# Kernel tuning notes

Hardware: AMD Instinct MI355X
Metric: run time of the kernel (lower is better)

## Reference

```python
import jax, jax.numpy as jnp
import numpy as np

HEAD_DIM = 128
N_HEADS = 32
N_KV = 8
EPS = 1e-6


def setup_inputs() -> dict:
    key = jax.random.key(0)
    ks = jax.random.split(key, 8)
    B, S, H = 1, 2048, 2560
    hidden_states = jax.random.normal(ks[0], (B, S, H), dtype=jnp.float32)
    # rotary embeddings (any values work for a math reference)
    pos = jnp.arange(S, dtype=jnp.float32)[:, None]
    inv_freq = 1.0 / (10000.0 ** (jnp.arange(0, HEAD_DIM, 2, dtype=jnp.float32) / HEAD_DIM))
    ang = pos * inv_freq[None, :]            # [S, HEAD_DIM/2]
    emb = jnp.concatenate([ang, ang], axis=-1)  # [S, HEAD_DIM]
    cos = jnp.cos(emb)[None]                 # [1, S, HEAD_DIM]
    sin = jnp.sin(emb)[None]
    sc = 0.02
    Wq = jax.random.normal(ks[1], (N_HEADS * HEAD_DIM, H), dtype=jnp.float32) * sc
    Wk = jax.random.normal(ks[2], (N_KV * HEAD_DIM, H), dtype=jnp.float32) * sc
    Wv = jax.random.normal(ks[3], (N_KV * HEAD_DIM, H), dtype=jnp.float32) * sc
    Wo = jax.random.normal(ks[4], (H, N_HEADS * HEAD_DIM), dtype=jnp.float32) * sc
    q_norm_w = jnp.ones((HEAD_DIM,), dtype=jnp.float32)
    k_norm_w = jnp.ones((HEAD_DIM,), dtype=jnp.float32)
    return dict(hidden_states=hidden_states, cos=cos, sin=sin,
                Wq=Wq, Wk=Wk, Wv=Wv, Wo=Wo,
                q_norm_w=q_norm_w, k_norm_w=k_norm_w)


def _rms_norm(x, w):
    var = jnp.mean(x * x, axis=-1, keepdims=True)
    return x * jax.lax.rsqrt(var + EPS) * w


def _rotate_half(x):
    x1, x2 = jnp.split(x, 2, axis=-1)
    return jnp.concatenate([-x2, x1], axis=-1)


def reference(hidden_states, cos, sin, Wq, Wk, Wv, Wo, q_norm_w, k_norm_w):
    B, S, H = hidden_states.shape
    scale = HEAD_DIM ** -0.5
    # projections -> [B, heads, S, D]
    q = (hidden_states @ Wq.T).reshape(B, S, N_HEADS, HEAD_DIM)
    k = (hidden_states @ Wk.T).reshape(B, S, N_KV, HEAD_DIM)
    v = (hidden_states @ Wv.T).reshape(B, S, N_KV, HEAD_DIM)
    q = _rms_norm(q, q_norm_w).transpose(0, 2, 1, 3)   # [B, 32, S, D]
    k = _rms_norm(k, k_norm_w).transpose(0, 2, 1, 3)   # [B, 8, S, D]
    v = v.transpose(0, 2, 1, 3)
    # RoPE (cos/sin broadcast over heads via [:, None])
    c = cos[:, None]
    s = sin[:, None]
    q = q * c + _rotate_half(q) * s
    k = k * c + _rotate_half(k) * s
    # GQA: expand kv heads (repeat_kv)
    rep = N_HEADS // N_KV
    k = jnp.repeat(k, rep, axis=1)  # [B, 32, S, D]
    v = jnp.repeat(v, rep, axis=1)
    # causal SDPA (prefill => is_causal=True, full-length cache)
    scores = jnp.einsum('bhqd,bhkd->bhqk', q, k) * scale
    causal = jnp.tril(jnp.ones((S, S), dtype=bool))
    scores = jnp.where(causal, scores, jnp.finfo(scores.dtype).min)
    probs = jax.nn.softmax(scores, axis=-1)
    out = jnp.einsum('bhqk,bhkd->bhqd', probs, v)      # [B, 32, S, D]
    out = out.transpose(0, 2, 1, 3).reshape(B, S, N_HEADS * HEAD_DIM)
    return out @ Wo.T
```

## Files before the change

### kernel.cpp

```cpp
#include <hip/hip_runtime.h>
#include <hip/hip_bf16.h>

#define S_LEN   2048
#define HID     2560
#define NH      32
#define NKV     8
#define HD      128
#define QDIM    (NH*HD)
#define KVDIM   (NKV*HD)

typedef __attribute__((ext_vector_type(8))) short short8;
typedef __attribute__((ext_vector_type(4))) float f32x4;

__device__ __forceinline__ unsigned short f2bf(float f) {
    unsigned u = __float_as_uint(f);
    u += 0x7fffu + ((u >> 16) & 1u);
    return (unsigned short)(u >> 16);
}
__device__ __forceinline__ float bf2f(unsigned short s) {
    return __uint_as_float(((unsigned)s) << 16);
}
__device__ __forceinline__ unsigned pk2bf(float a, float b) {
    __hip_bfloat162 h = __float22bfloat162_rn(make_float2(a, b));
    union { __hip_bfloat162 h; unsigned u; } c; c.h = h; return c.u;
}
__device__ __forceinline__ void gload16(const void* g, void* l) {
    __builtin_amdgcn_global_load_lds(
        (const __attribute__((address_space(1))) unsigned int*)g,
        (__attribute__((address_space(3))) unsigned int*)l, 16, 0, 0);
}

#define N4_HS  (S_LEN*HID/4)
#define N4_WQ  (QDIM*HID/4)
#define N4_WKV (KVDIM*HID/4)
__global__ __launch_bounds__(256) void cvt4(
    const float* __restrict__ hs, const float* __restrict__ Wq,
    const float* __restrict__ Wk, const float* __restrict__ Wv,
    unsigned short* __restrict__ hsB, unsigned short* __restrict__ WqB,
    unsigned short* __restrict__ WkB, unsigned short* __restrict__ WvB)
{
    int i = blockIdx.x * 256 + threadIdx.x;
    const float* s; unsigned short* d;
    if (i < N4_HS)                          { s = hs; d = hsB; }
    else if (i < N4_HS + N4_WQ)             { i -= N4_HS; s = Wq; d = WqB; }
    else if (i < N4_HS + N4_WQ + N4_WKV)    { i -= N4_HS + N4_WQ; s = Wk; d = WkB; }
    else                                    { i -= N4_HS + N4_WQ + N4_WKV; s = Wv; d = WvB; }
    float4 v = ((const float4*)s)[i];
    uint2 o;
    o.x = pk2bf(v.x, v.y); o.y = pk2bf(v.z, v.w);
    ((uint2*)d)[i] = o;
}

__global__ __launch_bounds__(256) void cvt_f32_bf16(
    const float* __restrict__ s, unsigned short* __restrict__ d, int n4)
{
    int i = blockIdx.x * 256 + threadIdx.x;
    if (i >= n4) return;
    float4 v = ((const float4*)s)[i];
    uint2 o;
    o.x = pk2bf(v.x, v.y); o.y = pk2bf(v.z, v.w);
    ((uint2*)d)[i] = o;
}

#define STG_A(b, h, t) do {                                                  \
    _Pragma("unroll")                                                        \
    for (int c_ = 0; c_ < 2; c_++) {                                         \
        int r_ = c_*128 + (h)*64 + (tid >> 3);                               \
        int cg_ = (tid & 7) ^ (r_ & 7);                                      \
        gload16(Ag + (size_t)(rowA0 + r_) * HID + (size_t)(t)*64 + cg_*8,    \
                &As[b][r_*64 + (tid & 7)*8]);                                \
    } } while (0)

#define STG_B(b, h, t) do {                                                  \
    _Pragma("unroll")                                                        \
    for (int c_ = 0; c_ < 2; c_++) {                                         \
        int r_ = c_*128 + ((tid >> 8) << 6) + (h)*32 + ((tid >> 3) & 31);    \
        int cg_ = (tid & 7) ^ (r_ & 7);                                      \
        gload16(Bg + (size_t)(rowB0 + r_) * HID + (size_t)(t)*64 + cg_*8,    \
                &Bs[b][r_*64 + (tid & 7)*8]);                                \
    } } while (0)

#define PHASE(b, rh, ch, STAGE_STMT, WV) do {                                \
    short8 af_[4][2], bf_[2][2];                                             \
    _Pragma("unroll")                                                        \
    for (int i_ = 0; i_ < 4; i_++) {                                         \
        int row_ = wr + (rh)*64 + i_*16 + l15;                               \
        _Pragma("unroll")                                                    \
        for (int kk_ = 0; kk_ < 2; kk_++)                                    \
            af_[i_][kk_] = *(const short8*)                                  \
                &As[b][row_*64 + (((kk_*4 + l4) ^ sw8))*8];                  \
    }                                                                        \
    _Pragma("unroll")                                                        \
    for (int j_ = 0; j_ < 2; j_++) {                                         \
        int row_ = wc + (ch)*32 + j_*16 + l15;                               \
        _Pragma("unroll")                                                    \
        for (int kk_ = 0; kk_ < 2; kk_++)                                    \
            bf_[j_][kk_] = *(const short8*)                                  \
                &Bs[b][row_*64 + (((kk_*4 + l4) ^ sw8))*8];                  \
    }                                                                        \
    STAGE_STMT;                                                              \
    asm volatile("s_barrier" ::: "memory");                                  \
    asm volatile("s_waitcnt lgkmcnt(0)" ::: "memory");                       \
    __builtin_amdgcn_s_setprio(1);                                           \
    _Pragma("unroll")                                                        \
    for (int kk_ = 0; kk_ < 2; kk_++)                                        \
        _Pragma("unroll")                                                    \
        for (int i_ = 0; i_ < 4; i_++)                                       \
            _Pragma("unroll")                                                \
            for (int j_ = 0; j_ < 2; j_++)                                   \
                acc[(rh)*4 + i_][(ch)*2 + j_] =                              \
                    __builtin_amdgcn_mfma_f32_16x16x32_bf16(                 \
                        af_[i_][kk_], bf_[j_][kk_],                          \
                        acc[(rh)*4 + i_][(ch)*2 + j_], 0, 0, 0);             \
    __builtin_amdgcn_s_setprio(0);                                           \
    if ((WV) == 1) {                                                         \
        if (p2v) asm volatile("s_waitcnt vmcnt(4)" ::: "memory");            \
        else     asm volatile("s_waitcnt vmcnt(0)" ::: "memory");            \
    } else if ((WV) == 2) {                                                  \
        asm volatile("s_waitcnt vmcnt(4)" ::: "memory");                     \
    }                                                                        \
    asm volatile("s_barrier" ::: "memory");                                  \
} while (0)

__global__ __launch_bounds__(512, 2) void gemm_qkv(
    const unsigned short* __restrict__ A,
    const unsigned short* __restrict__ Wq, const unsigned short* __restrict__ Wk,
    const unsigned short* __restrict__ Wv,
    unsigned short* __restrict__ Qo, unsigned short* __restrict__ Ko,
    unsigned short* __restrict__ VTo)
{
    __shared__ unsigned short As[2][256*64];
    __shared__ unsigned short Bs[2][256*64];

    const int flat = blockIdx.y * 24 + blockIdx.x;
    const int swz  = (flat & 7) * 24 + (flat >> 3);
    const int bx = swz % 24, by = swz / 24;

    const unsigned short* Bg; int rowB0;
    if (bx < 16)      { Bg = Wq; rowB0 = bx * 256; }
    else if (bx < 20) { Bg = Wk; rowB0 = (bx-16) * 256; }
    else              { Bg = Wv; rowB0 = (bx-20) * 256; }
    const unsigned short* Ag = A;
    const int rowA0 = by * 256;

    const int tid = threadIdx.x;
    const int lane = tid & 63, w = tid >> 6;
    const int l15 = lane & 15, l4 = lane >> 4;
    const int wr = (w >> 2) * 128;
    const int wc = (w & 3) * 64;
    const int sw8 = l15 & 7;

    f32x4 acc[8][4];
#pragma unroll
    for (int i = 0; i < 8; i++)
#pragma unroll
        for (int j = 0; j < 4; j++) acc[i][j] = (f32x4){0.f, 0.f, 0.f, 0.f};

    STG_A(0,0,0); STG_B(0,0,0); STG_A(0,1,0); STG_B(0,1,0);
    STG_A(1,0,1); STG_B(1,0,1);
    asm volatile("s_waitcnt vmcnt(4)" ::: "memory");
    asm volatile("s_barrier" ::: "memory");

#pragma unroll 1
    for (int t = 0; t < HID/64; t += 2) {
        const bool p2v = (t + 2 < HID/64);
        const bool p3v = (t + 3 < HID/64);
        PHASE(0, 0, 0, { STG_A(1,1,t+1); STG_B(1,1,t+1); }, 0);
        PHASE(0, 0, 1, {}, 0);
        PHASE(0, 1, 0, { if (p2v) STG_A(0,0,t+2); }, 0);
        PHASE(0, 1, 1, { if (p2v) STG_B(0,0,t+2); }, 1);
        PHASE(1, 0, 0, { if (p2v) { STG_A(0,1,t+2); STG_B(0,1,t+2); } }, 0);
        PHASE(1, 0, 1, {}, 0);
        PHASE(1, 1, 0, { if (p3v) STG_A(1,0,t+3); }, 0);
        PHASE(1, 1, 1, { if (p3v) STG_B(1,0,t+3); }, 2);
    }

    if (bx < 20) {
        unsigned short* C; int ldc, cb;
        if (bx < 16) { C = Qo; ldc = QDIM;  cb = bx*256; }
        else         { C = Ko; ldc = KVDIM; cb = (bx-16)*256; }
#pragma unroll
        for (int i = 0; i < 8; i++)
#pragma unroll
            for (int j = 0; j < 4; j++) {
                int row0 = by*256 + wr + i*16 + l4*4;
                int col  = cb + wc + j*16 + l15;
#pragma unroll
                for (int r = 0; r < 4; r++)
                    C[(size_t)(row0 + r) * ldc + col] = f2bf(acc[i][j][r]);
            }
    } else {
        const int cbase = (bx - 20) * 256;
#pragma unroll
        for (int i = 0; i < 8; i++)
#pragma unroll
            for (int j = 0; j < 4; j++) {
                int col  = cbase + wc + j*16 + l15;
                int row0 = by*256 + wr + i*16 + l4*4;
                int kvhh = col >> 7, d = col & 127;
                unsigned short* p = VTo + (size_t)kvhh*HD*S_LEN + (size_t)d*S_LEN + row0;
                uint2 pk;
                pk.x = pk2bf(acc[i][j][0], acc[i][j][1]);
                pk.y = pk2bf(acc[i][j][2], acc[i][j][3]);
                *(uint2*)p = pk;
            }
    }
}

__global__ __launch_bounds__(256) void gemm_out(
    const unsigned short* __restrict__ A, const unsigned short* __restrict__ B,
    float* __restrict__ C, int N, int Kd)
{
    __shared__ unsigned short As[64*64];
    __shared__ unsigned short Bs[128*64];
    const int tid = threadIdx.x;
    const int lane = tid & 63, w = tid >> 6;
    const int l15 = lane & 15, l4 = lane >> 4;
    const int wr = (w >> 1) * 32, wc = (w & 1) * 64;
    const int rowA0 = blockIdx.y * 64, rowB0 = blockIdx.x * 128;
    const int sw = l15 & 7;

    f32x4 acc[2][4];
#pragma unroll
    for (int i = 0; i < 2; i++)
#pragma unroll
        for (int j = 0; j < 4; j++) acc[i][j] = (f32x4){0.f, 0.f, 0.f, 0.f};

    for (int k0 = 0; k0 < Kd; k0 += 64) {
        __syncthreads();
#pragma unroll
        for (int i = 0; i < 2; i++) {
            int tc = tid + i * 256;
            int r = tc >> 3, cl = tc & 7;
            int cg = cl ^ (r & 7);
            gload16(A + (size_t)(rowA0 + r) * Kd + k0 + cg * 8, &As[tc * 8]);
        }
#pragma unroll
        for (int i = 0; i < 4; i++) {
            int tc = tid + i * 256;
            int r = tc >> 3, cl = tc & 7;
            int cg = cl ^ (r & 7);
            gload16(B + (size_t)(rowB0 + r) * Kd + k0 + cg * 8, &Bs[tc * 8]);
        }
        __syncthreads();

#pragma unroll
        for (int ks = 0; ks < 2; ks++) {
            const int kc = (ks * 4 + l4) ^ sw;
            short8 af[2], bf[4];
#pragma unroll
            for (int i = 0; i < 2; i++)
                af[i] = *(const short8*)&As[(wr + i*16 + l15)*64 + kc*8];
#pragma unroll
            for (int j = 0; j < 4; j++)
                bf[j] = *(const short8*)&Bs[(wc + j*16 + l15)*64 + kc*8];
#pragma unroll
            for (int i = 0; i < 2; i++)
#pragma unroll
                for (int j = 0; j < 4; j++)
                    acc[i][j] = __builtin_amdgcn_mfma_f32_16x16x32_bf16(
                        af[i], bf[j], acc[i][j], 0, 0, 0);
        }
    }

#pragma unroll
    for (int i = 0; i < 2; i++)
#pragma unroll
        for (int j = 0; j < 4; j++) {
            int row0 = rowA0 + wr + i*16 + l4*4;
            int col  = rowB0 + wc + j*16 + l15;
#pragma unroll
            for (int r = 0; r < 4; r++)
                C[(size_t)(row0 + r) * N + col] = acc[i][j][r];
        }
}

__global__ __launch_bounds__(256) void rmsnorm_rope_bf16(
    unsigned short* __restrict__ X, const float* __restrict__ w,
    const float* __restrict__ ct, const float* __restrict__ st, int nheads)
{
    int wid  = (blockIdx.x * blockDim.x + threadIdx.x) >> 6;
    int lane = threadIdx.x & 63;
    int s = wid / nheads;
    int h = wid - s * nheads;
    unsigned short* x = X + (size_t)s * (nheads * HD) + h * HD;

    float x1 = bf2f(x[lane]);
    float x2 = bf2f(x[lane + 64]);
    float ss = x1*x1 + x2*x2;
#pragma unroll
    for (int off = 32; off > 0; off >>= 1) ss += __shfl_xor(ss, off, 64);
    float r = rsqrtf(ss * (1.0f/128.0f) + 1e-6f);
    float n1 = x1 * r * w[lane];
    float n2 = x2 * r * w[lane + 64];
    float c1 = ct[s*HD + lane],      s1 = st[s*HD + lane];
    float c2 = ct[s*HD + lane + 64], s2 = st[s*HD + lane + 64];
    x[lane]      = f2bf(n1*c1 - n2*s1);
    x[lane + 64] = f2bf(n2*c2 + n1*s2);
}

__global__ __launch_bounds__(256, 3) void flash_mfma(
    const unsigned short* __restrict__ Q, const unsigned short* __restrict__ K,
    const unsigned short* __restrict__ VT, unsigned short* __restrict__ O)
{
    const int pb = blockIdx.x;
    const int h = blockIdx.y, kvh = h >> 2;
    const int tid = threadIdx.x;
    const int w = tid >> 6, lane = tid & 63;
    const int l15 = lane & 15, l4 = lane >> 4;

    __shared__ unsigned short Ks[64*128];
    __shared__ unsigned short Vt[128*64];
    __shared__ unsigned short Ps[4*16*72];
    __shared__ float Lw[4][16];

    const float scale2 = 0.08838834764831845f * 1.4426950408889634f;
    const float M2 = 17.3f;
    unsigned short* Pw = &Ps[w * 16 * 72];
    const unsigned short* VTh = VT + (size_t)kvh * HD * S_LEN;

#pragma unroll 1
    for (int phase = 0; phase < 2; phase++) {
        const int qt = phase ? pb : (31 - pb);
        const int q0 = qt * 64;

        short8 qa[4];
        {
            const unsigned short* qg = Q + (size_t)(q0 + w*16 + l15) * QDIM + h * HD;
#pragma unroll
            for (int ka = 0; ka < 4; ka++)
                qa[ka] = *(const short8*)(qg + ka*32 + l4*8);
        }

        const f32x4 zero = {0.f, 0.f, 0.f, 0.f};
        f32x4 accO[8];
#pragma unroll
        for (int j = 0; j < 8; j++) accO[j] = zero;
        float lsum = 0.f;

        for (int t = 0; t <= qt; t++) {
            const int c0 = t * 64;
            __syncthreads();
            {
#pragma unroll
                for (int i = 0; i < 4; i++) {
                    int tc = tid + i * 256;
                    int r = tc >> 4, cl = tc & 15;
                    int cg = cl ^ (r & 7);
                    gload16(K + (size_t)(c0 + r) * KVDIM + kvh * HD + cg * 8,
                            &Ks[tc * 8]);
                }
            }
            {
#pragma unroll
                for (int i = 0; i < 4; i++) {
                    int tc = tid + i * 256;
                    int r = tc >> 3, cl = tc & 7;
                    int cg = cl ^ (r & 7);
                    gload16(VTh + (size_t)r * S_LEN + c0 + cg * 8, &Vt[tc * 8]);
                }
            }
            __syncthreads();

            f32x4 sc[4];
#pragma unroll
            for (int mt = 0; mt < 4; mt++) sc[mt] = zero;
#pragma unroll
            for (int ka = 0; ka < 4; ka++) {
#pragma unroll
                for (int mt = 0; mt < 4; mt++) {
                    int row = mt*16 + l15;
                    int cs = (ka*4 + l4) ^ (row & 7);
                    short8 kb = *(const short8*)&Ks[row*128 + cs*8];
                    sc[mt] = __builtin_amdgcn_mfma_f32_16x16x32_bf16(kb, qa[ka], sc[mt], 0, 0, 0);
                }
            }

            const int qglob = q0 + w*16 + l15;
            const bool diag = (t == qt);
#pragma unroll
            for (int mt = 0; mt < 4; mt++) {
                float pv[4];
#pragma unroll
                for (int r = 0; r < 4; r++) {
                    int kvg = c0 + mt*16 + l4*4 + r;
                    float e = __builtin_amdgcn_exp2f(fmaf(sc[mt][r], scale2, -M2));
                    pv[r] = (!diag || kvg <= qglob) ? e : 0.f;
                    lsum += pv[r];
                }
                uint2 pk;
                pk.x = pk2bf(pv[0], pv[1]);
                pk.y = pk2bf(pv[2], pv[3]);
                *(uint2*)&Pw[l15*72 + mt*16 + l4*4] = pk;
            }

#pragma unroll
            for (int ks = 0; ks < 2; ks++) {
                short8 pf = *(const short8*)&Pw[l15*72 + ks*32 + l4*8];
                const int cs = (ks*4 + l4) ^ (l15 & 7);
#pragma unroll
                for (int dt = 0; dt < 8; dt++) {
                    short8 vf = *(const short8*)&Vt[(dt*16 + l15)*64 + cs*8];
                    accO[dt] = __builtin_amdgcn_mfma_f32_16x16x32_bf16(pf, vf, accO[dt], 0, 0, 0);
                }
            }
        }

        lsum += __shfl_xor(lsum, 16, 64);
        lsum += __shfl_xor(lsum, 32, 64);
        if (l4 == 0) Lw[w][l15] = lsum;
        f32x4 linv;
#pragma unroll
        for (int r = 0; r < 4; r++) linv[r] = 1.0f / Lw[w][l4*4 + r];

#pragma unroll
        for (int dt = 0; dt < 8; dt++)
#pragma unroll
            for (int r = 0; r < 4; r++) {
                int row_l = w*16 + l4*4 + r;
                O[(size_t)(q0 + row_l) * QDIM + h*HD + dt*16 + l15] =
                    f2bf(accO[dt][r] * linv[r]);
            }
    }
}

extern "C" void kernel_launch(void* const* d_in, const int* in_sizes, int n_in,
                              void* d_out, int out_size, void* d_ws, size_t ws_size,
                              hipStream_t stream)
{
    const float* hs   = (const float*)d_in[0];
    const float* cosb = (const float*)d_in[1];
    const float* sinb = (const float*)d_in[2];
    const float* Wq   = (const float*)d_in[3];
    const float* Wk   = (const float*)d_in[4];
    const float* Wv   = (const float*)d_in[5];
    const float* Wo   = (const float*)d_in[6];
    const float* qw   = (const float*)d_in[7];
    const float* kw   = (const float*)d_in[8];
    float* out = (float*)d_out;

    char* ws = (char*)d_ws;
    unsigned short* hsB = (unsigned short*)(ws);
    unsigned short* WqB = (unsigned short*)(ws + 10485760);
    unsigned short* WkB = (unsigned short*)(ws + 31457280);
    unsigned short* WvB = (unsigned short*)(ws + 36700160);
    unsigned short* KB  = (unsigned short*)(ws + 41943040);
    unsigned short* VT  = (unsigned short*)(ws + 46137344);
    unsigned short* WoB = (unsigned short*)(ws + 41943040);
    unsigned short* QB  = (unsigned short*)(ws + 62914560);
    unsigned short* CB  = (unsigned short*)(ws + 18874368);

    {
        int n4 = N4_HS + N4_WQ + 2 * N4_WKV;
        cvt4<<<(n4+255)/256, 256, 0, stream>>>(hs, Wq, Wk, Wv, hsB, WqB, WkB, WvB);
    }

    gemm_qkv<<<dim3(24, S_LEN/256), 512, 0, stream>>>(hsB, WqB, WkB, WvB, QB, KB, VT);

    rmsnorm_rope_bf16<<<S_LEN*NH/4,  256, 0, stream>>>(QB, qw, cosb, sinb, NH);
    rmsnorm_rope_bf16<<<S_LEN*NKV/4, 256, 0, stream>>>(KB, kw, cosb, sinb, NKV);

    flash_mfma<<<dim3(16, NH), 256, 0, stream>>>(QB, KB, VT, CB);

    cvt_f32_bf16<<<(HID*QDIM/4+255)/256, 256, 0, stream>>>(Wo, WoB, HID*QDIM/4);

    gemm_out<<<dim3(HID/128, S_LEN/64), 256, 0, stream>>>(CB, WoB, out, HID, QDIM);
}
```

Baseline: 402.7 us.

## Reuse B fragments across phases and deepen prefetch in QKV GEMM pipeline

Restructures the QKV GEMM main loop so each K-step loads B fragments into two persistent register sets and visits the quadrants in a serpentine order (00,01,11,10). Half of the LDS fragment reads are reused across phases instead of reloaded. The prefetch schedule now issues a whole K tile (both halves) one iteration earlier, with vmcnt(8) waits. The aim is to cut LDS read traffic and give global loads more latency slack, at the cost of extra fragment registers and more intricate barrier and waitcnt ordering.

```diff
diff --git a/kernel.cpp b/kernel.cpp
--- a/kernel.cpp
+++ b/kernel.cpp
@@ -80,28 +80,27 @@
                 &Bs[b][r_*64 + (tid & 7)*8]);                                \
     } } while (0)
 
-#define PHASE(b, rh, ch, STAGE_STMT, WV) do {                                \
-    short8 af_[4][2], bf_[2][2];                                             \
+#define LDA_(b, rh) do {                                                     \
     _Pragma("unroll")                                                        \
     for (int i_ = 0; i_ < 4; i_++) {                                         \
         int row_ = wr + (rh)*64 + i_*16 + l15;                               \
         _Pragma("unroll")                                                    \
         for (int kk_ = 0; kk_ < 2; kk_++)                                    \
-            af_[i_][kk_] = *(const short8*)                                  \
+            afr[i_][kk_] = *(const short8*)                                  \
                 &As[b][row_*64 + (((kk_*4 + l4) ^ sw8))*8];                  \
-    }                                                                        \
+    } } while (0)
+
+#define LDB_(b, ch, D) do {                                                  \
     _Pragma("unroll")                                                        \
     for (int j_ = 0; j_ < 2; j_++) {                                         \
         int row_ = wc + (ch)*32 + j_*16 + l15;                               \
         _Pragma("unroll")                                                    \
         for (int kk_ = 0; kk_ < 2; kk_++)                                    \
-            bf_[j_][kk_] = *(const short8*)                                  \
+            D[j_][kk_] = *(const short8*)                                    \
                 &Bs[b][row_*64 + (((kk_*4 + l4) ^ sw8))*8];                  \
-    }                                                                        \
-    STAGE_STMT;                                                              \
-    asm volatile("s_barrier" ::: "memory");                                  \
-    asm volatile("s_waitcnt lgkmcnt(0)" ::: "memory");                       \
-    __builtin_amdgcn_s_setprio(1);                                           \
+    } } while (0)
+
+#define MM_(rh, ch, D) do {                                                  \
     _Pragma("unroll")                                                        \
     for (int kk_ = 0; kk_ < 2; kk_++)                                        \
         _Pragma("unroll")                                                    \
@@ -110,17 +109,17 @@
             for (int j_ = 0; j_ < 2; j_++)                                   \
                 acc[(rh)*4 + i_][(ch)*2 + j_] =                              \
                     __builtin_amdgcn_mfma_f32_16x16x32_bf16(                 \
-                        af_[i_][kk_], bf_[j_][kk_],                          \
+                        afr[i_][kk_], D[j_][kk_],                            \
                         acc[(rh)*4 + i_][(ch)*2 + j_], 0, 0, 0);             \
-    __builtin_amdgcn_s_setprio(0);                                           \
-    if ((WV) == 1) {                                                         \
-        if (p2v) asm volatile("s_waitcnt vmcnt(4)" ::: "memory");            \
-        else     asm volatile("s_waitcnt vmcnt(0)" ::: "memory");            \
-    } else if ((WV) == 2) {                                                  \
-        asm volatile("s_waitcnt vmcnt(4)" ::: "memory");                     \
-    }                                                                        \
-    asm volatile("s_barrier" ::: "memory");                                  \
-} while (0)
+    } while (0)
+
+#define BAR_  asm volatile("s_barrier" ::: "memory")
+#define LG0_  asm volatile("s_waitcnt lgkmcnt(0)" ::: "memory")
+#define LG8_  asm volatile("s_waitcnt lgkmcnt(8)" ::: "memory")
+#define VM8_  asm volatile("s_waitcnt vmcnt(8)" ::: "memory")
+#define VM0_  asm volatile("s_waitcnt vmcnt(0)" ::: "memory")
+#define SP1_  __builtin_amdgcn_s_setprio(1)
+#define SP0_  __builtin_amdgcn_s_setprio(0)
 
 __global__ __launch_bounds__(512, 2) void gemm_qkv(
     const unsigned short* __restrict__ A,
@@ -156,23 +155,50 @@
 #pragma unroll
         for (int j = 0; j < 4; j++) acc[i][j] = (f32x4){0.f, 0.f, 0.f, 0.f};
 
-    STG_A(0,0,0); STG_B(0,0,0); STG_A(0,1,0); STG_B(0,1,0);
-    STG_A(1,0,1); STG_B(1,0,1);
-    asm volatile("s_waitcnt vmcnt(4)" ::: "memory");
-    asm volatile("s_barrier" ::: "memory");
+    short8 afr[4][2];
+    short8 b0r[2][2];
+    short8 b1r[2][2];
+
+    STG_A(0,0,0); STG_B(0,0,0); STG_B(0,1,0); STG_A(0,1,0);
+    STG_A(1,0,1); STG_B(1,0,1); STG_B(1,1,1); STG_A(1,1,1);
+    VM8_; BAR_;
 
 #pragma unroll 1
     for (int t = 0; t < HID/64; t += 2) {
         const bool p2v = (t + 2 < HID/64);
         const bool p3v = (t + 3 < HID/64);
-        PHASE(0, 0, 0, { STG_A(1,1,t+1); STG_B(1,1,t+1); }, 0);
-        PHASE(0, 0, 1, {}, 0);
-        PHASE(0, 1, 0, { if (p2v) STG_A(0,0,t+2); }, 0);
-        PHASE(0, 1, 1, { if (p2v) STG_B(0,0,t+2); }, 1);
-        PHASE(1, 0, 0, { if (p2v) { STG_A(0,1,t+2); STG_B(0,1,t+2); } }, 0);
-        PHASE(1, 0, 1, {}, 0);
-        PHASE(1, 1, 0, { if (p3v) STG_A(1,0,t+3); }, 0);
-        PHASE(1, 1, 1, { if (p3v) STG_B(1,0,t+3); }, 2);
+
+        LDA_(0,0); LDB_(0,0,b0r);
+        LG8_; BAR_; LG0_; SP1_; MM_(0,0,b0r); SP0_; BAR_;
+
+        LDB_(0,1,b1r);
+        if (p2v) { STG_A(0,0,t+2); STG_B(0,0,t+2); }
+        BAR_; LG0_; SP1_; MM_(0,1,b1r); SP0_; BAR_;
+
+        LDA_(0,1);
+        if (p2v) STG_B(0,1,t+2);
+        BAR_; LG0_; SP1_; MM_(1,1,b1r); SP0_; BAR_;
+
+        if (p2v) STG_A(0,1,t+2);
+        BAR_; SP1_; MM_(1,0,b0r); SP0_;
+        if (p2v) { VM8_; } else { VM0_; }
+        BAR_;
+
+        LDA_(1,0); LDB_(1,0,b0r);
+        LG8_; BAR_; LG0_; SP1_; MM_(0,0,b0r); SP0_; BAR_;
+
+        LDB_(1,1,b1r);
+        if (p3v) { STG_A(1,0,t+3); STG_B(1,0,t+3); }
+        BAR_; LG0_; SP1_; MM_(0,1,b1r); SP0_; BAR_;
+
+        LDA_(1,1);
+        if (p3v) STG_B(1,1,t+3);
+        BAR_; LG0_; SP1_; MM_(1,1,b1r); SP0_; BAR_;
+
+        if (p3v) STG_A(1,1,t+3);
+        BAR_; SP1_; MM_(1,0,b0r); SP0_;
+        if (p3v) { VM8_; }
+        BAR_;
     }
 
     if (bx < 20) {
```

New measurement: 385.8 us. 1.04x faster.
